# Performance work log

Measured on AMD Instinct MI355X. Metric: run time of the kernel, lower is better.

Reference implementation:

```python
import jax, jax.numpy as jnp
import numpy as np

B, L, H = 16, 512, 1024
K_START, K_END = 5, 5
LN_EPS = 1e-12
NEG = 1e30


def _layer_norm(x, gamma, beta):
    mu = jnp.mean(x, axis=-1, keepdims=True)
    var = jnp.mean(jnp.square(x - mu), axis=-1, keepdims=True)
    return (x - mu) * jax.lax.rsqrt(var + LN_EPS) * gamma + beta


def setup_inputs() -> dict:
    key = jax.random.key(0)
    ks = jax.random.split(key, 10)
    s = 0.02
    sequence_data = jax.random.normal(ks[0], (B, L, H), jnp.float32)
    class_index = jax.random.randint(ks[1], (B,), 0, L, dtype=jnp.int32)
    paragraph_mask = (jax.random.uniform(ks[2], (B, L)) > 0.1).astype(jnp.float32)
    paragraph_mask = paragraph_mask.at[:, 0].set(1.0)  # guarantee >=1 valid position per row
    return {
        'sequence_data': sequence_data,
        'class_index': class_index,
        'paragraph_mask': paragraph_mask,
        'W_start': jax.random.normal(ks[3], (H, 1), jnp.float32) * s,
        'b_start': jnp.zeros((1,), jnp.float32),
        'W_end_in': jax.random.normal(ks[4], (2 * H, H), jnp.float32) * s,
        'b_end_in': jnp.zeros((H,), jnp.float32),
        'ln_gamma': jnp.ones((H,), jnp.float32),
        'ln_beta': jnp.zeros((H,), jnp.float32),
        'W_end_out': jax.random.normal(ks[5], (H, 1), jnp.float32) * s,
        'b_end_out': jnp.zeros((1,), jnp.float32),
        'W_ans_in': jax.random.normal(ks[6], (2 * H, H), jnp.float32) * s,
        'b_ans_in': jnp.zeros((H,), jnp.float32),
        'W_ans_out': jax.random.normal(ks[7], (H, 1), jnp.float32) * s,
    }


def reference(sequence_data, class_index, paragraph_mask,
              W_start, b_start, W_end_in, b_end_in, ln_gamma, ln_beta,
              W_end_out, b_end_out, W_ans_in, b_ans_in, W_ans_out):
    mask = paragraph_mask  # [b, l] float, 1 = valid

    # ---- start logits ----
    start_logits = jnp.einsum('blh,ho->bl', sequence_data, W_start) + b_start[0]  # [b,l]
    masked_start_logits = start_logits * mask - NEG * (1.0 - mask)
    start_predictions = jax.nn.log_softmax(masked_start_logits, axis=-1)

    # ---- beam search over start positions (inference branch) ----
    start_top_predictions, start_top_index = jax.lax.top_k(start_predictions, K_START)  # [b,k]
    # one-hot einsum gather 'blh,bkl->bkh' expressed as direct indexing
    start_features = jnp.take_along_axis(sequence_data, start_top_index[:, :, None], axis=1)  # [b,k,h]

    # end_logits inner dense on concat([tiled seq, tiled start_features]) along h:
    # split the [2h, h] kernel and broadcast-add instead of materializing the tiled concat.
    W1, W2 = W_end_in[:H], W_end_in[H:]
    inner = jnp.tanh(
        jnp.einsum('blh,hd->bld', sequence_data, W1)[:, :, None, :]
        + jnp.einsum('bkh,hd->bkd', start_features, W2)[:, None, :, :]
        + b_end_in
    )  # [b,l,k,h]
    inner = _layer_norm(inner, ln_gamma, ln_beta)
    end_logits = jnp.einsum('blkh,ho->blk', inner, W_end_out) + b_end_out[0]  # [b,l,k]
    end_logits = jnp.transpose(end_logits, (0, 2, 1))  # [b,k,l]

    mask_k = mask[:, None, :]  # [b,1,l]
    masked_end_logits = end_logits * mask_k - NEG * (1.0 - mask_k)
    end_predictions = jax.nn.log_softmax(masked_end_logits, axis=-1)

    end_top_predictions, _end_top_index = jax.lax.top_k(end_predictions, K_END)  # [b,k,k2]
    end_top_predictions = end_top_predictions.reshape(-1, K_START * K_END)

    # ---- answer (class) logits ----
    class_feature = sequence_data[jnp.arange(sequence_data.shape[0]), class_index]  # [b,h]
    start_p = jax.nn.softmax(masked_start_logits, axis=-1)
    start_feature = jnp.einsum('blh,bl->bh', sequence_data, start_p)
    answer_feature = jnp.concatenate([start_feature, class_feature], axis=-1)  # [b,2h]
    answer_feature = jnp.tanh(answer_feature @ W_ans_in + b_ans_in)  # dropout is identity at inference
    class_logits = (answer_feature @ W_ans_out)[:, 0]  # [b]

    return (start_predictions, end_predictions, masked_start_logits, masked_end_logits,
            start_top_predictions, end_top_predictions, class_logits)
```

## Files before the change

### kernel.cpp

```cpp
#include <hip/hip_runtime.h>
#include <math.h>

#define HD   1024
#define LSEQ 512
#define NB   16
#define KTOP 5
#define NEGV 1e30f

typedef __bf16 bf16x8 __attribute__((ext_vector_type(8)));
typedef float  f32x4  __attribute__((ext_vector_type(4)));

__device__ inline unsigned short f2bf(float f) {
  unsigned u = __float_as_uint(f);
  unsigned r = (u + 0x7FFFu + ((u >> 16) & 1u)) >> 16;
  return (unsigned short)r;
}
__device__ inline float bf2f(unsigned short u) {
  return __uint_as_float(((unsigned)u) << 16);
}

__device__ inline float fast_tanh(float x) {
  float e = __expf(-2.f * fabsf(x));
  float v = (1.f - e) / (1.f + e);
  return copysignf(v, x);
}

__device__ inline float tanh_scaled(float xs) {
  float e = __builtin_amdgcn_exp2f(xs);
  float r = __builtin_amdgcn_rcpf(1.f + e);
  return fmaf(-2.f, r, 1.f);
}

#define GLDS(g, l) __builtin_amdgcn_global_load_lds(                      \
    (const __attribute__((address_space(1))) unsigned int*)(g),          \
    (__attribute__((address_space(3))) unsigned int*)(l), 16, 0, 0)

__global__ void k_prep(const float* __restrict__ seq,
                       unsigned short* __restrict__ seqb,
                       const float* __restrict__ Wst,
                       const float* __restrict__ bst,
                       const float* __restrict__ mask,
                       float* __restrict__ msl,
                       const float* __restrict__ Wei,
                       unsigned short* __restrict__ w1t,
                       const float* __restrict__ gam,
                       const float* __restrict__ bet,
                       const float* __restrict__ Weo,
                       const float* __restrict__ beo,
                       float* __restrict__ gw_ws,
                       float* __restrict__ sgb_ws) {
  __shared__ unsigned short tile[32][33];
  __shared__ float redp[4][2];
  int bx = blockIdx.x;
  if (bx < 2048) {
    int wave = threadIdx.x >> 6, lane = threadIdx.x & 63;
    int row = bx * 4 + wave;
    const float4* s4 = (const float4*)(seq + (size_t)row * HD);
    const float4* w4 = (const float4*)Wst;
    ushort4* o4 = (ushort4*)(seqb + (size_t)row * HD);
    float acc = 0.f;
#pragma unroll
    for (int m = 0; m < 4; ++m) {
      int i = lane + 64 * m;
      float4 a = s4[i], w = w4[i];
      acc += a.x * w.x + a.y * w.y + a.z * w.z + a.w * w.w;
      ushort4 o;
      o.x = f2bf(a.x); o.y = f2bf(a.y); o.z = f2bf(a.z); o.w = f2bf(a.w);
      o4[i] = o;
    }
#pragma unroll
    for (int off = 32; off; off >>= 1) acc += __shfl_xor(acc, off);
    if (lane == 0) {
      float logit = acc + bst[0];
      float mv = mask[row];
      msl[row] = logit * mv - NEGV * (1.f - mv);
    }
  } else if (bx < 3072) {
    int tb = bx - 2048;
    int h0 = (tb & 31) * 32, d0 = (tb >> 5) * 32;
    int tx = threadIdx.x & 31, ty = threadIdx.x >> 5;
#pragma unroll
    for (int i = 0; i < 4; ++i)
      tile[ty + 8 * i][tx] = f2bf(Wei[(size_t)(h0 + ty + 8 * i) * HD + d0 + tx]);
    __syncthreads();
#pragma unroll
    for (int i = 0; i < 4; ++i)
      w1t[(size_t)(d0 + ty + 8 * i) * HD + h0 + tx] = tile[tx][ty + 8 * i];
  } else {
    int t = threadIdx.x, wave = t >> 6, lane = t & 63;
    float4 g = ((const float4*)gam)[t];
    float4 w = ((const float4*)Weo)[t];
    float4 bv = ((const float4*)bet)[t];
    float4 gwv = make_float4(g.x * w.x, g.y * w.y, g.z * w.z, g.w * w.w);
    ((float4*)gw_ws)[t] = gwv;
    float pg = gwv.x + gwv.y + gwv.z + gwv.w;
    float pb = bv.x * w.x + bv.y * w.y + bv.z * w.z + bv.w * w.w;
#pragma unroll
    for (int off = 32; off; off >>= 1) {
      pg += __shfl_xor(pg, off);
      pb += __shfl_xor(pb, off);
    }
    if (lane == 0) { redp[wave][0] = pg; redp[wave][1] = pb; }
    __syncthreads();
    if (t == 0) {
      sgb_ws[0] = redp[0][0] + redp[1][0] + redp[2][0] + redp[3][0];
      sgb_ws[1] = redp[0][1] + redp[1][1] + redp[2][1] + redp[3][1] + beo[0];
    }
  }
}

__global__ void k_softmax_topk(const float* __restrict__ xin,
                               float* __restrict__ lsm_out,
                               float* __restrict__ top_out,
                               float* __restrict__ p_out,
                               int* __restrict__ idx_out) {
  int row = blockIdx.x, t = threadIdx.x;
  int lane = t & 63, wid = t >> 6;
  __shared__ float redf[4];
  __shared__ int redi[4];
  __shared__ float bc_m, bc_s;
  __shared__ int bc_i;
  const float* x = xin + (size_t)row * LSEQ;
  float x0 = x[t], x1 = x[t + 256];

  float m = fmaxf(x0, x1);
#pragma unroll
  for (int off = 32; off; off >>= 1) m = fmaxf(m, __shfl_xor(m, off));
  if (lane == 0) redf[wid] = m;
  __syncthreads();
  if (t == 0) bc_m = fmaxf(fmaxf(redf[0], redf[1]), fmaxf(redf[2], redf[3]));
  __syncthreads();
  m = bc_m;

  float e0 = expf(x0 - m), e1 = expf(x1 - m);
  float s = e0 + e1;
#pragma unroll
  for (int off = 32; off; off >>= 1) s += __shfl_xor(s, off);
  if (lane == 0) redf[wid] = s;
  __syncthreads();
  if (t == 0) bc_s = redf[0] + redf[1] + redf[2] + redf[3];
  __syncthreads();
  s = bc_s;
  float ls = logf(s);

  lsm_out[(size_t)row * LSEQ + t] = x0 - m - ls;
  lsm_out[(size_t)row * LSEQ + t + 256] = x1 - m - ls;
  if (p_out) {
    float inv = 1.f / s;
    p_out[(size_t)row * LSEQ + t] = e0 * inv;
    p_out[(size_t)row * LSEQ + t + 256] = e1 * inv;
  }

  bool a0 = true, a1 = true;
  for (int it = 0; it < KTOP; ++it) {
    float v0 = a0 ? x0 : -INFINITY;
    float v1 = a1 ? x1 : -INFINITY;
    float bv = v0; int bi = t;
    if (v1 > bv) { bv = v1; bi = t + 256; }
#pragma unroll
    for (int off = 32; off; off >>= 1) {
      float ov = __shfl_xor(bv, off);
      int oi = __shfl_xor(bi, off);
      if (ov > bv || (ov == bv && oi < bi)) { bv = ov; bi = oi; }
    }
    __syncthreads();
    if (lane == 0) { redf[wid] = bv; redi[wid] = bi; }
    __syncthreads();
    if (t == 0) {
      float wv = redf[0]; int wi = redi[0];
      for (int w = 1; w < 4; ++w)
        if (redf[w] > wv || (redf[w] == wv && redi[w] < wi)) { wv = redf[w]; wi = redi[w]; }
      top_out[row * KTOP + it] = wv - m - ls;
      if (idx_out) idx_out[row * KTOP + it] = wi;
      bc_i = wi;
    }
    __syncthreads();
    int wi = bc_i;
    if (wi == t) a0 = false;
    if (wi == t + 256) a1 = false;
  }
}

__global__ void k_x2p(const float* __restrict__ seq,
                      const int* __restrict__ idx,
                      const float* __restrict__ Wei,
                      float* __restrict__ x2part) {
  int bk = blockIdx.x, b = bk / KTOP, s = blockIdx.y, t = threadIdx.x;
  __shared__ float srow[128];
  int l = idx[bk];
  if (t < 128) srow[t] = seq[((size_t)(b * LSEQ + l)) * HD + s * 128 + t];
  __syncthreads();
  const float* W2 = Wei + (size_t)HD * HD + (size_t)s * 128 * HD;
  float4 acc = make_float4(0.f, 0.f, 0.f, 0.f);
#pragma unroll 8
  for (int h = 0; h < 128; ++h) {
    float4 wv = *(const float4*)(W2 + (size_t)h * HD + 4 * t);
    float sv = srow[h];
    acc.x = fmaf(sv, wv.x, acc.x);
    acc.y = fmaf(sv, wv.y, acc.y);
    acc.z = fmaf(sv, wv.z, acc.z);
    acc.w = fmaf(sv, wv.w, acc.w);
  }
  *(float4*)(x2part + ((size_t)bk * 8 + s) * HD + 4 * t) = acc;
}

__global__ void k_x2r(const float* __restrict__ x2part,
                      const float* __restrict__ bei,
                      float* __restrict__ x2p) {
  int bk = blockIdx.x, t = threadIdx.x;
  float4 a = *(const float4*)(bei + 4 * t);
#pragma unroll
  for (int s = 0; s < 8; ++s) {
    float4 p = *(const float4*)(x2part + ((size_t)bk * 8 + s) * HD + 4 * t);
    a.x += p.x; a.y += p.y; a.z += p.z; a.w += p.w;
  }
  *(float4*)(x2p + (size_t)bk * HD + 4 * t) = a;
}

__launch_bounds__(256, 2)
__global__ void k_gemm(const unsigned short* __restrict__ Abf,
                       const unsigned short* __restrict__ Bt,
                       unsigned short* __restrict__ X1) {
  __shared__ unsigned short As[2][128 * 64];
  __shared__ unsigned short Bs[2][128 * 64];
  int t = threadIdx.x;
  int w = t >> 6, lane = t & 63, ln = lane & 15, hi = lane >> 4;
  int wr = w >> 1, wc = w & 1;
  int R0 = blockIdx.x * 128, C0 = blockIdx.y * 128;

  f32x4 acc[4][4] = {};

#define STAGE(buf, kc)                                                        \
  do {                                                                        \
    _Pragma("unroll")                                                         \
    for (int p_ = 0; p_ < 4; ++p_) {                                          \
      int rr_ = p_ * 32 + (t >> 3);                                           \
      int cc_ = (t & 7) ^ (rr_ & 7);                                          \
      GLDS(Abf + (size_t)(R0 + rr_) * HD + (kc) + cc_ * 8,                    \
           &As[buf][p_ * 2048 + w * 512]);                                    \
      GLDS(Bt + (size_t)(C0 + rr_) * HD + (kc) + cc_ * 8,                     \
           &Bs[buf][p_ * 2048 + w * 512]);                                    \
    }                                                                         \
  } while (0)

  STAGE(0, 0);
  for (int it = 0; it < 16; ++it) {
    int cur = it & 1;
    if (it < 15) {
      STAGE(cur ^ 1, (it + 1) * 64);
      asm volatile("s_waitcnt vmcnt(8)" ::: "memory");
    } else {
      asm volatile("s_waitcnt vmcnt(0)" ::: "memory");
    }
    __builtin_amdgcn_s_barrier();
    __builtin_amdgcn_sched_barrier(0);
#pragma unroll
    for (int ks = 0; ks < 2; ++ks) {
      bf16x8 av[4], bv[4];
#pragma unroll
      for (int m = 0; m < 4; ++m) {
        int r = wr * 64 + m * 16 + ln;
        av[m] = *(const bf16x8*)(const void*)&As[cur][r * 64 + (((ks * 4 + hi) ^ (r & 7)) * 8)];
      }
#pragma unroll
      for (int n = 0; n < 4; ++n) {
        int r = wc * 64 + n * 16 + ln;
        bv[n] = *(const bf16x8*)(const void*)&Bs[cur][r * 64 + (((ks * 4 + hi) ^ (r & 7)) * 8)];
      }
#pragma unroll
      for (int m = 0; m < 4; ++m)
#pragma unroll
        for (int n = 0; n < 4; ++n)
          acc[m][n] = __builtin_amdgcn_mfma_f32_16x16x32_bf16(av[m], bv[n], acc[m][n], 0, 0, 0);
    }
    __builtin_amdgcn_sched_barrier(0);
    __builtin_amdgcn_s_barrier();
  }
#undef STAGE

#pragma unroll
  for (int m = 0; m < 4; ++m)
#pragma unroll
    for (int j = 0; j < 4; ++j) {
      int row = R0 + wr * 64 + m * 16 + hi * 4 + j;
#pragma unroll
      for (int n = 0; n < 4; ++n) {
        int col = C0 + wc * 64 + n * 16 + ln;
        X1[(size_t)row * HD + col] = f2bf(acc[m][n][j]);
      }
    }
}

__launch_bounds__(256)
__global__ void k_endrow(const unsigned short* __restrict__ X1,
                         const float* __restrict__ x2p,
                         const float* __restrict__ gw_ws,
                         const float* __restrict__ sgb_ws,
                         const float* __restrict__ mask,
                         float* __restrict__ mel) {
  __shared__ float x2s[KTOP * HD];
  const float A = 2.885390081777927f;
  int t = threadIdx.x, wave = t >> 6, lane = t & 63;
  int row = blockIdx.x * 4 + wave;
  int b = row >> 9, l = row & 511;

  {
    const float4* src = (const float4*)(x2p + (size_t)b * KTOP * HD);
    float4* dst = (float4*)x2s;
    for (int i = t; i < KTOP * HD / 4; i += 256) {
      float4 v = src[i];
      dst[i] = make_float4(v.x * A, v.y * A, v.z * A, v.w * A);
    }
  }

  float xs[16], gwr[16];
  const unsigned short* xrow = X1 + (size_t)row * HD + lane * 4;
#pragma unroll
  for (int q = 0; q < 4; ++q) {
    ushort4 u = *(const ushort4*)(xrow + q * 256);
    xs[4 * q + 0] = bf2f(u.x) * A;
    xs[4 * q + 1] = bf2f(u.y) * A;
    xs[4 * q + 2] = bf2f(u.z) * A;
    xs[4 * q + 3] = bf2f(u.w) * A;
    float4 g = *(const float4*)(gw_ws + q * 256 + lane * 4);
    gwr[4 * q + 0] = g.x; gwr[4 * q + 1] = g.y;
    gwr[4 * q + 2] = g.z; gwr[4 * q + 3] = g.w;
  }
  float mv = mask[row];
  float sG = sgb_ws[0], sBW = sgb_ws[1];
  __syncthreads();

#pragma unroll
  for (int k = 0; k < KTOP; ++k) {
    float sv = 0.f, s2 = 0.f, sg = 0.f;
#pragma unroll
    for (int q = 0; q < 4; ++q) {
      float4 xq = *(const float4*)&x2s[k * HD + q * 256 + lane * 4];
      float v0 = tanh_scaled(xs[4 * q + 0] + xq.x);
      float v1 = tanh_scaled(xs[4 * q + 1] + xq.y);
      float v2 = tanh_scaled(xs[4 * q + 2] + xq.z);
      float v3 = tanh_scaled(xs[4 * q + 3] + xq.w);
      sv += v0 + v1 + v2 + v3;
      s2 = fmaf(v0, v0, s2); s2 = fmaf(v1, v1, s2);
      s2 = fmaf(v2, v2, s2); s2 = fmaf(v3, v3, s2);
      sg = fmaf(v0, gwr[4 * q + 0], sg); sg = fmaf(v1, gwr[4 * q + 1], sg);
      sg = fmaf(v2, gwr[4 * q + 2], sg); sg = fmaf(v3, gwr[4 * q + 3], sg);
    }
#pragma unroll
    for (int off = 32; off; off >>= 1) {
      sv += __shfl_xor(sv, off);
      s2 += __shfl_xor(s2, off);
      sg += __shfl_xor(sg, off);
    }
    if (lane == 0) {
      float mu = sv * (1.f / (float)HD);
      float var = s2 * (1.f / (float)HD) - mu * mu;
      float rr = rsqrtf(var + 1e-12f);
      float logit = rr * (sg - mu * sG) + sBW;
      mel[((size_t)b * KTOP + k) * LSEQ + l] = logit * mv - NEGV * (1.f - mv);
    }
  }
}

__global__ void k_ans_in(const float* __restrict__ seq,
                         const float* __restrict__ p_ws,
                         const int* __restrict__ cls,
                         float* __restrict__ pa,
                         float* __restrict__ cf) {
  int b = blockIdx.x, s = blockIdx.y, t = threadIdx.x;
  __shared__ float ps[16];
  if (t < 16) ps[t] = p_ws[b * LSEQ + s * 16 + t];
  __syncthreads();
  const float* sb = seq + (size_t)(b * LSEQ + s * 16) * HD;
  float4 acc = make_float4(0.f, 0.f, 0.f, 0.f);
#pragma unroll
  for (int r = 0; r < 16; ++r) {
    float4 v = *(const float4*)(sb + (size_t)r * HD + 4 * t);
    float p = ps[r];
    acc.x = fmaf(p, v.x, acc.x);
    acc.y = fmaf(p, v.y, acc.y);
    acc.z = fmaf(p, v.z, acc.z);
    acc.w = fmaf(p, v.w, acc.w);
  }
  *(float4*)(pa + ((size_t)b * 32 + s) * HD + 4 * t) = acc;
  if (s == 0) {
    int ci = cls[b];
    *(float4*)(cf + (size_t)b * HD + 4 * t) =
        *(const float4*)(seq + (size_t)(b * LSEQ + ci) * HD + 4 * t);
  }
}

__global__ void k_ans_mid(const float* __restrict__ pa,
                          const float* __restrict__ cf,
                          const float* __restrict__ Wai,
                          float* __restrict__ pans) {
  int b = blockIdx.x, c = blockIdx.y, t = threadIdx.x;
  __shared__ float a_s[128];
  if (t < 128) {
    int i = c * 128 + t;
    float av;
    if (i < HD) {
      av = 0.f;
#pragma unroll
      for (int s = 0; s < 32; ++s) av += pa[((size_t)b * 32 + s) * HD + i];
    } else {
      av = cf[(size_t)b * HD + (i - HD)];
    }
    a_s[t] = av;
  }
  __syncthreads();
  float4 acc = make_float4(0.f, 0.f, 0.f, 0.f);
#pragma unroll 8
  for (int r = 0; r < 128; ++r) {
    float4 wv = *(const float4*)(Wai + (size_t)(c * 128 + r) * HD + 4 * t);
    float a = a_s[r];
    acc.x = fmaf(a, wv.x, acc.x);
    acc.y = fmaf(a, wv.y, acc.y);
    acc.z = fmaf(a, wv.z, acc.z);
    acc.w = fmaf(a, wv.w, acc.w);
  }
  *(float4*)(pans + ((size_t)b * 16 + c) * HD + 4 * t) = acc;
}

__global__ void k_ans_final(const float* __restrict__ pans,
                            const float* __restrict__ bai,
                            const float* __restrict__ Wao,
                            float* __restrict__ out6) {
  int b = blockIdx.x, t = threadIdx.x, lane = t & 63, wid = t >> 6;
  __shared__ float red[4];
  float4 a = *(const float4*)(bai + 4 * t);
#pragma unroll
  for (int c = 0; c < 16; ++c) {
    float4 p = *(const float4*)(pans + ((size_t)b * 16 + c) * HD + 4 * t);
    a.x += p.x; a.y += p.y; a.z += p.z; a.w += p.w;
  }
  float4 wo = *(const float4*)(Wao + 4 * t);
  float part = fast_tanh(a.x) * wo.x + fast_tanh(a.y) * wo.y +
               fast_tanh(a.z) * wo.z + fast_tanh(a.w) * wo.w;
#pragma unroll
  for (int off = 32; off; off >>= 1) part += __shfl_xor(part, off);
  if (lane == 0) red[wid] = part;
  __syncthreads();
  if (t == 0) out6[b] = red[0] + red[1] + red[2] + red[3];
}

__launch_bounds__(256, 2)
__global__ void k_gemm_end_at(const unsigned short* __restrict__ Abf,
                              const unsigned short* __restrict__ Bt,
                              const float* __restrict__ x2p,
                              const float* __restrict__ gamma,
                              const float* __restrict__ Wout,
                              float* __restrict__ outp) {
  __shared__ unsigned short As[2][128 * 64];
  __shared__ unsigned short Bs[2][128 * 64];
  int t = threadIdx.x;
  int w = t >> 6, lane = t & 63, ln = lane & 15, hi = lane >> 4;
  int wr = w >> 1, wc = w & 1;
  int R0 = blockIdx.x * 128, C0 = blockIdx.y * 128;
  int b = R0 >> 9;
  f32x4 acc[4][4] = {};
#define STAGE(buf, kc)                                                        \
  do {                                                                        \
    _Pragma("unroll")                                                         \
    for (int p_ = 0; p_ < 4; ++p_) {                                          \
      int rr_ = p_ * 32 + (t >> 3);                                           \
      int cc_ = (t & 7) ^ (rr_ & 7);                                          \
      GLDS(Abf + (size_t)(R0 + rr_) * HD + (kc) + cc_ * 8,                    \
           &As[buf][p_ * 2048 + w * 512]);                                    \
      GLDS(Bt + (size_t)(C0 + rr_) * HD + (kc) + cc_ * 8,                     \
           &Bs[buf][p_ * 2048 + w * 512]);                                    \
    }                                                                         \
  } while (0)
  STAGE(0, 0);
  for (int it = 0; it < 16; ++it) {
    int cur = it & 1;
    if (it < 15) {
      STAGE(cur ^ 1, (it + 1) * 64);
      asm volatile("s_waitcnt vmcnt(8)" ::: "memory");
    } else {
      asm volatile("s_waitcnt vmcnt(0)" ::: "memory");
    }
    __builtin_amdgcn_s_barrier();
    __builtin_amdgcn_sched_barrier(0);
#pragma unroll
    for (int ks = 0; ks < 2; ++ks) {
      bf16x8 av[4], bv[4];
#pragma unroll
      for (int m = 0; m < 4; ++m) {
        int r = wr * 64 + m * 16 + ln;
        av[m] = *(const bf16x8*)(const void*)&As[cur][r * 64 + (((ks * 4 + hi) ^ (r & 7)) * 8)];
      }
#pragma unroll
      for (int n = 0; n < 4; ++n) {
        int r = wc * 64 + n * 16 + ln;
        bv[n] = *(const bf16x8*)(const void*)&Bs[cur][r * 64 + (((ks * 4 + hi) ^ (r & 7)) * 8)];
      }
#pragma unroll
      for (int m = 0; m < 4; ++m)
#pragma unroll
        for (int n = 0; n < 4; ++n)
          acc[m][n] = __builtin_amdgcn_mfma_f32_16x16x32_bf16(av[m], bv[n], acc[m][n], 0, 0, 0);
    }
    __builtin_amdgcn_sched_barrier(0);
    __builtin_amdgcn_s_barrier();
  }
#undef STAGE
  float gsv[4];
  float x2v[4][KTOP];
#pragma unroll
  for (int n = 0; n < 4; ++n) {
    int c = C0 + wc * 64 + n * 16 + ln;
    gsv[n] = gamma[c] * Wout[c];
#pragma unroll
    for (int k = 0; k < KTOP; ++k) x2v[n][k] = x2p[((size_t)b * KTOP + k) * HD + c];
  }
#pragma unroll
  for (int m = 0; m < 4; ++m)
#pragma unroll
    for (int j = 0; j < 4; ++j) {
      int row = R0 + wr * 64 + m * 16 + hi * 4 + j;
#pragma unroll
      for (int k = 0; k < KTOP; ++k) {
        float sv = 0.f, s2 = 0.f, sg = 0.f;
#pragma unroll
        for (int n = 0; n < 4; ++n) {
          float v = fast_tanh(acc[m][n][j] + x2v[n][k]);
          sv += v; s2 += v * v; sg += v * gsv[n];
        }
#pragma unroll
        for (int off = 8; off; off >>= 1) {
          sv += __shfl_xor(sv, off);
          s2 += __shfl_xor(s2, off);
          sg += __shfl_xor(sg, off);
        }
        if (ln == 0) {
          float* p = outp + ((size_t)row * KTOP + k) * 3;
          atomicAdd(p, sv);
          atomicAdd(p + 1, s2);
          atomicAdd(p + 2, sg);
        }
      }
    }
}

__global__ void k_end_final(const float* __restrict__ sums,
                            const float* __restrict__ gamma,
                            const float* __restrict__ beta,
                            const float* __restrict__ Wout,
                            const float* __restrict__ beo,
                            const float* __restrict__ mask,
                            float* __restrict__ mel) {
  int bk = blockIdx.x, b = bk / KTOP, k = bk % KTOP;
  int t = threadIdx.x, lane = t & 63, wid = t >> 6;
  __shared__ float red[4][2];
  float pg = 0.f, pb = 0.f;
  for (int i = t; i < HD; i += 256) {
    float wv = Wout[i];
    pg += gamma[i] * wv;
    pb += beta[i] * wv;
  }
#pragma unroll
  for (int off = 32; off; off >>= 1) {
    pg += __shfl_xor(pg, off);
    pb += __shfl_xor(pb, off);
  }
  if (lane == 0) { red[wid][0] = pg; red[wid][1] = pb; }
  __syncthreads();
  float sG = red[0][0] + red[1][0] + red[2][0] + red[3][0];
  float sBW = red[0][1] + red[1][1] + red[2][1] + red[3][1] + beo[0];
  for (int l = t; l < LSEQ; l += 256) {
    int row = b * LSEQ + l;
    const float* s = sums + ((size_t)row * KTOP + k) * 3;
    float sv = s[0], s2 = s[1], sg = s[2];
    float mu = sv * (1.f / (float)HD);
    float var = s2 * (1.f / (float)HD) - mu * mu;
    float rr = rsqrtf(var + 1e-12f);
    float logit = rr * (sg - mu * sG) + sBW;
    float mv = mask[row];
    mel[((size_t)b * KTOP + k) * LSEQ + l] = logit * mv - NEGV * (1.f - mv);
  }
}

extern "C" void kernel_launch(void* const* d_in, const int* in_sizes, int n_in,
                              void* d_out, int out_size, void* d_ws, size_t ws_size,
                              hipStream_t stream) {
  (void)in_sizes; (void)n_in; (void)out_size;
  const float* seq = (const float*)d_in[0];
  const int*   cls = (const int*)d_in[1];
  const float* mask = (const float*)d_in[2];
  const float* Wst = (const float*)d_in[3];
  const float* bst = (const float*)d_in[4];
  const float* Wei = (const float*)d_in[5];
  const float* bei = (const float*)d_in[6];
  const float* gam = (const float*)d_in[7];
  const float* bet = (const float*)d_in[8];
  const float* Weo = (const float*)d_in[9];
  const float* beo = (const float*)d_in[10];
  const float* Wai = (const float*)d_in[11];
  const float* bai = (const float*)d_in[12];
  const float* Wao = (const float*)d_in[13];

  float* out = (float*)d_out;
  float* out0 = out;
  float* out1 = out0 + 8192;
  float* out2 = out1 + 40960;
  float* out3 = out2 + 8192;
  float* out4 = out3 + 40960;
  float* out5 = out4 + 80;
  float* out6 = out5 + 400;

  char* p = (char*)d_ws;
  unsigned short* seqb = (unsigned short*)p;  p += (size_t)8192 * 1024 * 2;
  unsigned short* w1t  = (unsigned short*)p;  p += (size_t)1024 * 1024 * 2;
  float* p_ws   = (float*)p;                  p += 8192 * 4;
  int*   idx_ws = (int*)p;                    p += 128 * 4;
  float* x2p    = (float*)p;                  p += (size_t)80 * 1024 * 4;
  float* gw_ws  = (float*)p;                  p += 1024 * 4;
  float* sgb_ws = (float*)p;                  p += 4 * 4;
  float* pa     = (float*)p;                  p += (size_t)16 * 32 * 1024 * 4;
  float* cf     = (float*)p;                  p += (size_t)16 * 1024 * 4;
  float* pans   = (float*)p;                  p += (size_t)16 * 16 * 1024 * 4;
  float* x2part = (float*)p;
  unsigned short* x1 = (unsigned short*)p;
  float* sums = (float*)(p + (size_t)640 * 1024 * 4);
  size_t base = (size_t)(p - (char*)d_ws);
  size_t need_big = base + (size_t)8192 * 1024 * 2;
  size_t need_small = base + (size_t)640 * 1024 * 4 + (size_t)8192 * KTOP * 3 * 4;

  k_prep<<<3073, 256, 0, stream>>>(seq, seqb, Wst, bst, mask, out2, Wei, w1t,
                                   gam, bet, Weo, beo, gw_ws, sgb_ws);
  k_softmax_topk<<<NB, 256, 0, stream>>>(out2, out0, out4, p_ws, idx_ws);
  k_x2p<<<dim3(NB * KTOP, 8), 256, 0, stream>>>(seq, idx_ws, Wei, x2part);
  k_x2r<<<NB * KTOP, 256, 0, stream>>>(x2part, bei, x2p);

  if (ws_size >= need_big) {
    k_gemm<<<dim3(64, 8), 256, 0, stream>>>(seqb, w1t, x1);
    k_endrow<<<2048, 256, 0, stream>>>(x1, x2p, gw_ws, sgb_ws, mask, out3);
  } else if (ws_size >= need_small) {
    hipMemsetAsync(sums, 0, (size_t)8192 * KTOP * 3 * sizeof(float), stream);
    k_gemm_end_at<<<dim3(64, 8), 256, 0, stream>>>(seqb, w1t, x2p, gam, Weo, sums);
    k_end_final<<<NB * KTOP, 256, 0, stream>>>(sums, gam, bet, Weo, beo, mask, out3);
  }

  k_softmax_topk<<<NB * KTOP, 256, 0, stream>>>(out3, out1, out5, nullptr, nullptr);
  k_ans_in<<<dim3(NB, 32), 256, 0, stream>>>(seq, p_ws, cls, pa, cf);
  k_ans_mid<<<dim3(NB, 16), 256, 0, stream>>>(pa, cf, Wai, pans);
  k_ans_final<<<NB, 256, 0, stream>>>(pans, bai, Wao, out6);
}
```

Measured before the change: 105.4 us.

## Merge independent kernels into horizontally fused launches with atomic x2 accumulation

```diff
diff --git a/kernel.cpp b/kernel.cpp
--- a/kernel.cpp
+++ b/kernel.cpp
@@ -34,6 +34,334 @@
 #define GLDS(g, l) __builtin_amdgcn_global_load_lds(                      \
     (const __attribute__((address_space(1))) unsigned int*)(g),          \
     (__attribute__((address_space(3))) unsigned int*)(l), 16, 0, 0)
+
+
+__device__ __forceinline__ void sm_body(int row, const float* __restrict__ xin,
+                                        float* __restrict__ lsm_out,
+                                        float* __restrict__ top_out,
+                                        float* __restrict__ p_out,
+                                        int* __restrict__ idx_out) {
+  __shared__ float redf[4];
+  __shared__ int redi[4];
+  __shared__ float bc_m, bc_s;
+  __shared__ int bc_i;
+  int t = threadIdx.x, lane = t & 63, wid = t >> 6;
+  const float* x = xin + (size_t)row * LSEQ;
+  float x0 = x[t], x1 = x[t + 256];
+
+  float m = fmaxf(x0, x1);
+#pragma unroll
+  for (int off = 32; off; off >>= 1) m = fmaxf(m, __shfl_xor(m, off));
+  if (lane == 0) redf[wid] = m;
+  __syncthreads();
+  if (t == 0) bc_m = fmaxf(fmaxf(redf[0], redf[1]), fmaxf(redf[2], redf[3]));
+  __syncthreads();
+  m = bc_m;
+
+  float e0 = expf(x0 - m), e1 = expf(x1 - m);
+  float s = e0 + e1;
+#pragma unroll
+  for (int off = 32; off; off >>= 1) s += __shfl_xor(s, off);
+  if (lane == 0) redf[wid] = s;
+  __syncthreads();
+  if (t == 0) bc_s = redf[0] + redf[1] + redf[2] + redf[3];
+  __syncthreads();
+  s = bc_s;
+  float ls = logf(s);
+
+  lsm_out[(size_t)row * LSEQ + t] = x0 - m - ls;
+  lsm_out[(size_t)row * LSEQ + t + 256] = x1 - m - ls;
+  if (p_out) {
+    float inv = 1.f / s;
+    p_out[(size_t)row * LSEQ + t] = e0 * inv;
+    p_out[(size_t)row * LSEQ + t + 256] = e1 * inv;
+  }
+
+  bool a0 = true, a1 = true;
+  for (int it = 0; it < KTOP; ++it) {
+    float v0 = a0 ? x0 : -INFINITY;
+    float v1 = a1 ? x1 : -INFINITY;
+    float bv = v0; int bi = t;
+    if (v1 > bv) { bv = v1; bi = t + 256; }
+#pragma unroll
+    for (int off = 32; off; off >>= 1) {
+      float ov = __shfl_xor(bv, off);
+      int oi = __shfl_xor(bi, off);
+      if (ov > bv || (ov == bv && oi < bi)) { bv = ov; bi = oi; }
+    }
+    __syncthreads();
+    if (lane == 0) { redf[wid] = bv; redi[wid] = bi; }
+    __syncthreads();
+    if (t == 0) {
+      float wv = redf[0]; int wi = redi[0];
+      for (int w = 1; w < 4; ++w)
+        if (redf[w] > wv || (redf[w] == wv && redi[w] < wi)) { wv = redf[w]; wi = redi[w]; }
+      top_out[row * KTOP + it] = wv - m - ls;
+      if (idx_out) idx_out[row * KTOP + it] = wi;
+      bc_i = wi;
+    }
+    __syncthreads();
+    int wi = bc_i;
+    if (wi == t) a0 = false;
+    if (wi == t + 256) a1 = false;
+  }
+}
+
+__device__ __forceinline__ void gemm_body(int gid,
+                                          const unsigned short* __restrict__ Abf,
+                                          const unsigned short* __restrict__ Bt,
+                                          unsigned short* __restrict__ X1) {
+  __shared__ unsigned short SH[32768];
+  unsigned short* As = SH;
+  unsigned short* Bs = SH + 16384;
+  int t = threadIdx.x;
+  int w = t >> 6, lane = t & 63, ln = lane & 15, hi = lane >> 4;
+  int wr = w >> 1, wc = w & 1;
+  int R0 = (gid >> 3) * 128, C0 = (gid & 7) * 128;
+
+  f32x4 acc[4][4] = {};
+
+#define STAGE(buf, kc)                                                        \
+  do {                                                                        \
+    _Pragma("unroll")                                                         \
+    for (int p_ = 0; p_ < 4; ++p_) {                                          \
+      int rr_ = p_ * 32 + (t >> 3);                                           \
+      int cc_ = (t & 7) ^ (rr_ & 7);                                          \
+      GLDS(Abf + (size_t)(R0 + rr_) * HD + (kc) + cc_ * 8,                    \
+           As + (buf) * 8192 + p_ * 2048 + w * 512);                          \
+      GLDS(Bt + (size_t)(C0 + rr_) * HD + (kc) + cc_ * 8,                     \
+           Bs + (buf) * 8192 + p_ * 2048 + w * 512);                          \
+    }                                                                         \
+  } while (0)
+
+  STAGE(0, 0);
+  for (int it = 0; it < 16; ++it) {
+    int cur = it & 1;
+    if (it < 15) {
+      STAGE(cur ^ 1, (it + 1) * 64);
+      asm volatile("s_waitcnt vmcnt(8)" ::: "memory");
+    } else {
+      asm volatile("s_waitcnt vmcnt(0)" ::: "memory");
+    }
+    __builtin_amdgcn_s_barrier();
+    __builtin_amdgcn_sched_barrier(0);
+#pragma unroll
+    for (int ks = 0; ks < 2; ++ks) {
+      bf16x8 av[4], bv[4];
+#pragma unroll
+      for (int m = 0; m < 4; ++m) {
+        int r = wr * 64 + m * 16 + ln;
+        av[m] = *(const bf16x8*)(const void*)&As[cur * 8192 + r * 64 + (((ks * 4 + hi) ^ (r & 7)) * 8)];
+      }
+#pragma unroll
+      for (int n = 0; n < 4; ++n) {
+        int r = wc * 64 + n * 16 + ln;
+        bv[n] = *(const bf16x8*)(const void*)&Bs[cur * 8192 + r * 64 + (((ks * 4 + hi) ^ (r & 7)) * 8)];
+      }
+#pragma unroll
+      for (int m = 0; m < 4; ++m)
+#pragma unroll
+        for (int n = 0; n < 4; ++n)
+          acc[m][n] = __builtin_amdgcn_mfma_f32_16x16x32_bf16(av[m], bv[n], acc[m][n], 0, 0, 0);
+    }
+    __builtin_amdgcn_sched_barrier(0);
+    __builtin_amdgcn_s_barrier();
+  }
+#undef STAGE
+
+#pragma unroll
+  for (int m = 0; m < 4; ++m)
+#pragma unroll
+    for (int j = 0; j < 4; ++j) {
+      int row = R0 + wr * 64 + m * 16 + hi * 4 + j;
+#pragma unroll
+      for (int n = 0; n < 4; ++n) {
+        int col = C0 + wc * 64 + n * 16 + ln;
+        X1[(size_t)row * HD + col] = f2bf(acc[m][n][j]);
+      }
+    }
+}
+
+__device__ __forceinline__ void x2slice_body(int q, const float* __restrict__ seq,
+                                             const int* __restrict__ idx,
+                                             const float* __restrict__ Wei,
+                                             float* __restrict__ x2p) {
+  __shared__ float srow[128];
+  int bk = q >> 3, s = q & 7, t = threadIdx.x;
+  int b = bk / KTOP;
+  int l = idx[bk];
+  if (t < 128) srow[t] = seq[((size_t)(b * LSEQ + l)) * HD + s * 128 + t];
+  __syncthreads();
+  const float* W2 = Wei + (size_t)HD * HD + (size_t)s * 128 * HD;
+  float4 acc = make_float4(0.f, 0.f, 0.f, 0.f);
+#pragma unroll 8
+  for (int h = 0; h < 128; ++h) {
+    float4 wv = *(const float4*)(W2 + (size_t)h * HD + 4 * t);
+    float sv = srow[h];
+    acc.x = fmaf(sv, wv.x, acc.x);
+    acc.y = fmaf(sv, wv.y, acc.y);
+    acc.z = fmaf(sv, wv.z, acc.z);
+    acc.w = fmaf(sv, wv.w, acc.w);
+  }
+  float* dst = x2p + (size_t)bk * HD + 4 * t;
+  atomicAdd(dst + 0, acc.x);
+  atomicAdd(dst + 1, acc.y);
+  atomicAdd(dst + 2, acc.z);
+  atomicAdd(dst + 3, acc.w);
+}
+
+__device__ __forceinline__ void ansin_body(int q, const float* __restrict__ seq,
+                                           const float* __restrict__ p_ws,
+                                           const int* __restrict__ cls,
+                                           float* __restrict__ pa,
+                                           float* __restrict__ cf) {
+  __shared__ float ps[16];
+  int b = q >> 5, s = q & 31, t = threadIdx.x;
+  if (t < 16) ps[t] = p_ws[b * LSEQ + s * 16 + t];
+  __syncthreads();
+  const float* sb = seq + (size_t)(b * LSEQ + s * 16) * HD;
+  float4 acc = make_float4(0.f, 0.f, 0.f, 0.f);
+#pragma unroll
+  for (int r = 0; r < 16; ++r) {
+    float4 v = *(const float4*)(sb + (size_t)r * HD + 4 * t);
+    float p = ps[r];
+    acc.x = fmaf(p, v.x, acc.x);
+    acc.y = fmaf(p, v.y, acc.y);
+    acc.z = fmaf(p, v.z, acc.z);
+    acc.w = fmaf(p, v.w, acc.w);
+  }
+  *(float4*)(pa + ((size_t)b * 32 + s) * HD + 4 * t) = acc;
+  if (s == 0) {
+    int ci = cls[b];
+    *(float4*)(cf + (size_t)b * HD + 4 * t) =
+        *(const float4*)(seq + (size_t)(b * LSEQ + ci) * HD + 4 * t);
+  }
+}
+
+__device__ __forceinline__ void endrow_body(int bx, const unsigned short* __restrict__ X1,
+                                            const float* __restrict__ x2p,
+                                            const float* __restrict__ gw_ws,
+                                            const float* __restrict__ sgb_ws,
+                                            const float* __restrict__ mask,
+                                            float* __restrict__ mel) {
+  __shared__ float x2s[KTOP * HD];
+  const float A = 2.885390081777927f;
+  int t = threadIdx.x, wave = t >> 6, lane = t & 63;
+  int row = bx * 4 + wave;
+  int b = row >> 9, l = row & 511;
+
+  {
+    const float4* src = (const float4*)(x2p + (size_t)b * KTOP * HD);
+    float4* dst = (float4*)x2s;
+    for (int i = t; i < KTOP * HD / 4; i += 256) {
+      float4 v = src[i];
+      dst[i] = make_float4(v.x * A, v.y * A, v.z * A, v.w * A);
+    }
+  }
+
+  float xs[16], gwr[16];
+  const unsigned short* xrow = X1 + (size_t)row * HD + lane * 4;
+#pragma unroll
+  for (int q = 0; q < 4; ++q) {
+    ushort4 u = *(const ushort4*)(xrow + q * 256);
+    xs[4 * q + 0] = bf2f(u.x) * A;
+    xs[4 * q + 1] = bf2f(u.y) * A;
+    xs[4 * q + 2] = bf2f(u.z) * A;
+    xs[4 * q + 3] = bf2f(u.w) * A;
+    float4 g = *(const float4*)(gw_ws + q * 256 + lane * 4);
+    gwr[4 * q + 0] = g.x; gwr[4 * q + 1] = g.y;
+    gwr[4 * q + 2] = g.z; gwr[4 * q + 3] = g.w;
+  }
+  float mv = mask[row];
+  float sG = sgb_ws[0], sBW = sgb_ws[1];
+  __syncthreads();
+
+#pragma unroll
+  for (int k = 0; k < KTOP; ++k) {
+    float sv = 0.f, s2 = 0.f, sg = 0.f;
+#pragma unroll
+    for (int q = 0; q < 4; ++q) {
+      float4 xq = *(const float4*)&x2s[k * HD + q * 256 + lane * 4];
+      float v0 = tanh_scaled(xs[4 * q + 0] + xq.x);
+      float v1 = tanh_scaled(xs[4 * q + 1] + xq.y);
+      float v2 = tanh_scaled(xs[4 * q + 2] + xq.z);
+      float v3 = tanh_scaled(xs[4 * q + 3] + xq.w);
+      sv += v0 + v1 + v2 + v3;
+      s2 = fmaf(v0, v0, s2); s2 = fmaf(v1, v1, s2);
+      s2 = fmaf(v2, v2, s2); s2 = fmaf(v3, v3, s2);
+      sg = fmaf(v0, gwr[4 * q + 0], sg); sg = fmaf(v1, gwr[4 * q + 1], sg);
+      sg = fmaf(v2, gwr[4 * q + 2], sg); sg = fmaf(v3, gwr[4 * q + 3], sg);
+    }
+#pragma unroll
+    for (int off = 32; off; off >>= 1) {
+      sv += __shfl_xor(sv, off);
+      s2 += __shfl_xor(s2, off);
+      sg += __shfl_xor(sg, off);
+    }
+    if (lane == 0) {
+      float mu = sv * (1.f / (float)HD);
+      float var = s2 * (1.f / (float)HD) - mu * mu;
+      float rr = rsqrtf(var + 1e-12f);
+      float logit = rr * (sg - mu * sG) + sBW;
+      mel[((size_t)b * KTOP + k) * LSEQ + l] = logit * mv - NEGV * (1.f - mv);
+    }
+  }
+}
+
+__device__ __forceinline__ void ansmid_body(int q, const float* __restrict__ pa,
+                                            const float* __restrict__ cf,
+                                            const float* __restrict__ Wai,
+                                            float* __restrict__ pans) {
+  __shared__ float a_s[128];
+  int b = q >> 4, c = q & 15, t = threadIdx.x;
+  if (t < 128) {
+    int i = c * 128 + t;
+    float av;
+    if (i < HD) {
+      av = 0.f;
+#pragma unroll
+      for (int s = 0; s < 32; ++s) av += pa[((size_t)b * 32 + s) * HD + i];
+    } else {
+      av = cf[(size_t)b * HD + (i - HD)];
+    }
+    a_s[t] = av;
+  }
+  __syncthreads();
+  float4 acc = make_float4(0.f, 0.f, 0.f, 0.f);
+#pragma unroll 8
+  for (int r = 0; r < 128; ++r) {
+    float4 wv = *(const float4*)(Wai + (size_t)(c * 128 + r) * HD + 4 * t);
+    float a = a_s[r];
+    acc.x = fmaf(a, wv.x, acc.x);
+    acc.y = fmaf(a, wv.y, acc.y);
+    acc.z = fmaf(a, wv.z, acc.z);
+    acc.w = fmaf(a, wv.w, acc.w);
+  }
+  *(float4*)(pans + ((size_t)b * 16 + c) * HD + 4 * t) = acc;
+}
+
+__device__ __forceinline__ void ansfinal_body(int b, const float* __restrict__ pans,
+                                              const float* __restrict__ bai,
+                                              const float* __restrict__ Wao,
+                                              float* __restrict__ out6) {
+  __shared__ float red[4];
+  int t = threadIdx.x, lane = t & 63, wid = t >> 6;
+  float4 a = *(const float4*)(bai + 4 * t);
+#pragma unroll
+  for (int c = 0; c < 16; ++c) {
+    float4 p = *(const float4*)(pans + ((size_t)b * 16 + c) * HD + 4 * t);
+    a.x += p.x; a.y += p.y; a.z += p.z; a.w += p.w;
+  }
+  float4 wo = *(const float4*)(Wao + 4 * t);
+  float part = fast_tanh(a.x) * wo.x + fast_tanh(a.y) * wo.y +
+               fast_tanh(a.z) * wo.z + fast_tanh(a.w) * wo.w;
+#pragma unroll
+  for (int off = 32; off; off >>= 1) part += __shfl_xor(part, off);
+  if (lane == 0) red[wid] = part;
+  __syncthreads();
+  if (t == 0) out6[b] = red[0] + red[1] + red[2] + red[3];
+}
+
 
 __global__ void k_prep(const float* __restrict__ seq,
                        unsigned short* __restrict__ seqb,
@@ -48,7 +376,9 @@
                        const float* __restrict__ Weo,
                        const float* __restrict__ beo,
                        float* __restrict__ gw_ws,
-                       float* __restrict__ sgb_ws) {
+                       float* __restrict__ sgb_ws,
+                       const float* __restrict__ bei,
+                       float* __restrict__ x2p) {
   __shared__ unsigned short tile[32][33];
   __shared__ float redp[4][2];
   int bx = blockIdx.x;
@@ -86,7 +416,7 @@
 #pragma unroll
     for (int i = 0; i < 4; ++i)
       w1t[(size_t)(d0 + ty + 8 * i) * HD + h0 + tx] = tile[tx][ty + 8 * i];
-  } else {
+  } else if (bx == 3072) {
     int t = threadIdx.x, wave = t >> 6, lane = t & 63;
     float4 g = ((const float4*)gam)[t];
     float4 w = ((const float4*)Weo)[t];
@@ -106,6 +436,9 @@
       sgb_ws[0] = redp[0][0] + redp[1][0] + redp[2][0] + redp[3][0];
       sgb_ws[1] = redp[0][1] + redp[1][1] + redp[2][1] + redp[3][1] + beo[0];
     }
+  } else {
+    int row = bx - 3073;
+    ((float4*)(x2p + (size_t)row * HD))[threadIdx.x] = ((const float4*)bei)[threadIdx.x];
   }
 }
 
@@ -114,334 +447,67 @@
                                float* __restrict__ top_out,
                                float* __restrict__ p_out,
                                int* __restrict__ idx_out) {
-  int row = blockIdx.x, t = threadIdx.x;
-  int lane = t & 63, wid = t >> 6;
-  __shared__ float redf[4];
-  __shared__ int redi[4];
-  __shared__ float bc_m, bc_s;
-  __shared__ int bc_i;
-  const float* x = xin + (size_t)row * LSEQ;
-  float x0 = x[t], x1 = x[t + 256];
-
-  float m = fmaxf(x0, x1);
-#pragma unroll
-  for (int off = 32; off; off >>= 1) m = fmaxf(m, __shfl_xor(m, off));
-  if (lane == 0) redf[wid] = m;
-  __syncthreads();
-  if (t == 0) bc_m = fmaxf(fmaxf(redf[0], redf[1]), fmaxf(redf[2], redf[3]));
-  __syncthreads();
-  m = bc_m;
-
-  float e0 = expf(x0 - m), e1 = expf(x1 - m);
-  float s = e0 + e1;
-#pragma unroll
-  for (int off = 32; off; off >>= 1) s += __shfl_xor(s, off);
-  if (lane == 0) redf[wid] = s;
-  __syncthreads();
-  if (t == 0) bc_s = redf[0] + redf[1] + redf[2] + redf[3];
-  __syncthreads();
-  s = bc_s;
-  float ls = logf(s);
-
-  lsm_out[(size_t)row * LSEQ + t] = x0 - m - ls;
-  lsm_out[(size_t)row * LSEQ + t + 256] = x1 - m - ls;
-  if (p_out) {
-    float inv = 1.f / s;
-    p_out[(size_t)row * LSEQ + t] = e0 * inv;
-    p_out[(size_t)row * LSEQ + t + 256] = e1 * inv;
-  }
-
-  bool a0 = true, a1 = true;
-  for (int it = 0; it < KTOP; ++it) {
-    float v0 = a0 ? x0 : -INFINITY;
-    float v1 = a1 ? x1 : -INFINITY;
-    float bv = v0; int bi = t;
-    if (v1 > bv) { bv = v1; bi = t + 256; }
-#pragma unroll
-    for (int off = 32; off; off >>= 1) {
-      float ov = __shfl_xor(bv, off);
-      int oi = __shfl_xor(bi, off);
-      if (ov > bv || (ov == bv && oi < bi)) { bv = ov; bi = oi; }
-    }
-    __syncthreads();
-    if (lane == 0) { redf[wid] = bv; redi[wid] = bi; }
-    __syncthreads();
-    if (t == 0) {
-      float wv = redf[0]; int wi = redi[0];
-      for (int w = 1; w < 4; ++w)
-        if (redf[w] > wv || (redf[w] == wv && redi[w] < wi)) { wv = redf[w]; wi = redi[w]; }
-      top_out[row * KTOP + it] = wv - m - ls;
-      if (idx_out) idx_out[row * KTOP + it] = wi;
-      bc_i = wi;
-    }
-    __syncthreads();
-    int wi = bc_i;
-    if (wi == t) a0 = false;
-    if (wi == t + 256) a1 = false;
-  }
-}
-
-__global__ void k_x2p(const float* __restrict__ seq,
+  sm_body(blockIdx.x, xin, lsm_out, top_out, p_out, idx_out);
+}
+
+__launch_bounds__(256, 2)
+__global__ void k_big(const unsigned short* __restrict__ Abf,
+                      const unsigned short* __restrict__ Bt,
+                      unsigned short* __restrict__ X1,
+                      const float* __restrict__ seq,
                       const int* __restrict__ idx,
                       const float* __restrict__ Wei,
-                      float* __restrict__ x2part) {
-  int bk = blockIdx.x, b = bk / KTOP, s = blockIdx.y, t = threadIdx.x;
-  __shared__ float srow[128];
-  int l = idx[bk];
-  if (t < 128) srow[t] = seq[((size_t)(b * LSEQ + l)) * HD + s * 128 + t];
-  __syncthreads();
-  const float* W2 = Wei + (size_t)HD * HD + (size_t)s * 128 * HD;
-  float4 acc = make_float4(0.f, 0.f, 0.f, 0.f);
-#pragma unroll 8
-  for (int h = 0; h < 128; ++h) {
-    float4 wv = *(const float4*)(W2 + (size_t)h * HD + 4 * t);
-    float sv = srow[h];
-    acc.x = fmaf(sv, wv.x, acc.x);
-    acc.y = fmaf(sv, wv.y, acc.y);
-    acc.z = fmaf(sv, wv.z, acc.z);
-    acc.w = fmaf(sv, wv.w, acc.w);
-  }
-  *(float4*)(x2part + ((size_t)bk * 8 + s) * HD + 4 * t) = acc;
-}
-
-__global__ void k_x2r(const float* __restrict__ x2part,
-                      const float* __restrict__ bei,
-                      float* __restrict__ x2p) {
-  int bk = blockIdx.x, t = threadIdx.x;
-  float4 a = *(const float4*)(bei + 4 * t);
-#pragma unroll
-  for (int s = 0; s < 8; ++s) {
-    float4 p = *(const float4*)(x2part + ((size_t)bk * 8 + s) * HD + 4 * t);
-    a.x += p.x; a.y += p.y; a.z += p.z; a.w += p.w;
-  }
-  *(float4*)(x2p + (size_t)bk * HD + 4 * t) = a;
-}
-
-__launch_bounds__(256, 2)
-__global__ void k_gemm(const unsigned short* __restrict__ Abf,
-                       const unsigned short* __restrict__ Bt,
-                       unsigned short* __restrict__ X1) {
-  __shared__ unsigned short As[2][128 * 64];
-  __shared__ unsigned short Bs[2][128 * 64];
-  int t = threadIdx.x;
-  int w = t >> 6, lane = t & 63, ln = lane & 15, hi = lane >> 4;
-  int wr = w >> 1, wc = w & 1;
-  int R0 = blockIdx.x * 128, C0 = blockIdx.y * 128;
-
-  f32x4 acc[4][4] = {};
-
-#define STAGE(buf, kc)                                                        \
-  do {                                                                        \
-    _Pragma("unroll")                                                         \
-    for (int p_ = 0; p_ < 4; ++p_) {                                          \
-      int rr_ = p_ * 32 + (t >> 3);                                           \
-      int cc_ = (t & 7) ^ (rr_ & 7);                                          \
-      GLDS(Abf + (size_t)(R0 + rr_) * HD + (kc) + cc_ * 8,                    \
-           &As[buf][p_ * 2048 + w * 512]);                                    \
-      GLDS(Bt + (size_t)(C0 + rr_) * HD + (kc) + cc_ * 8,                     \
-           &Bs[buf][p_ * 2048 + w * 512]);                                    \
-    }                                                                         \
-  } while (0)
-
-  STAGE(0, 0);
-  for (int it = 0; it < 16; ++it) {
-    int cur = it & 1;
-    if (it < 15) {
-      STAGE(cur ^ 1, (it + 1) * 64);
-      asm volatile("s_waitcnt vmcnt(8)" ::: "memory");
-    } else {
-      asm volatile("s_waitcnt vmcnt(0)" ::: "memory");
-    }
-    __builtin_amdgcn_s_barrier();
-    __builtin_amdgcn_sched_barrier(0);
-#pragma unroll
-    for (int ks = 0; ks < 2; ++ks) {
-      bf16x8 av[4], bv[4];
-#pragma unroll
-      for (int m = 0; m < 4; ++m) {
-        int r = wr * 64 + m * 16 + ln;
-        av[m] = *(const bf16x8*)(const void*)&As[cur][r * 64 + (((ks * 4 + hi) ^ (r & 7)) * 8)];
-      }
-#pragma unroll
-      for (int n = 0; n < 4; ++n) {
-        int r = wc * 64 + n * 16 + ln;
-        bv[n] = *(const bf16x8*)(const void*)&Bs[cur][r * 64 + (((ks * 4 + hi) ^ (r & 7)) * 8)];
-      }
-#pragma unroll
-      for (int m = 0; m < 4; ++m)
-#pragma unroll
-        for (int n = 0; n < 4; ++n)
-          acc[m][n] = __builtin_amdgcn_mfma_f32_16x16x32_bf16(av[m], bv[n], acc[m][n], 0, 0, 0);
-    }
-    __builtin_amdgcn_sched_barrier(0);
-    __builtin_amdgcn_s_barrier();
-  }
-#undef STAGE
-
-#pragma unroll
-  for (int m = 0; m < 4; ++m)
-#pragma unroll
-    for (int j = 0; j < 4; ++j) {
-      int row = R0 + wr * 64 + m * 16 + hi * 4 + j;
-#pragma unroll
-      for (int n = 0; n < 4; ++n) {
-        int col = C0 + wc * 64 + n * 16 + ln;
-        X1[(size_t)row * HD + col] = f2bf(acc[m][n][j]);
-      }
-    }
-}
-
-__launch_bounds__(256)
-__global__ void k_endrow(const unsigned short* __restrict__ X1,
-                         const float* __restrict__ x2p,
-                         const float* __restrict__ gw_ws,
-                         const float* __restrict__ sgb_ws,
-                         const float* __restrict__ mask,
-                         float* __restrict__ mel) {
-  __shared__ float x2s[KTOP * HD];
-  const float A = 2.885390081777927f;
-  int t = threadIdx.x, wave = t >> 6, lane = t & 63;
-  int row = blockIdx.x * 4 + wave;
-  int b = row >> 9, l = row & 511;
-
-  {
-    const float4* src = (const float4*)(x2p + (size_t)b * KTOP * HD);
-    float4* dst = (float4*)x2s;
-    for (int i = t; i < KTOP * HD / 4; i += 256) {
-      float4 v = src[i];
-      dst[i] = make_float4(v.x * A, v.y * A, v.z * A, v.w * A);
-    }
-  }
-
-  float xs[16], gwr[16];
-  const unsigned short* xrow = X1 + (size_t)row * HD + lane * 4;
-#pragma unroll
-  for (int q = 0; q < 4; ++q) {
-    ushort4 u = *(const ushort4*)(xrow + q * 256);
-    xs[4 * q + 0] = bf2f(u.x) * A;
-    xs[4 * q + 1] = bf2f(u.y) * A;
-    xs[4 * q + 2] = bf2f(u.z) * A;
-    xs[4 * q + 3] = bf2f(u.w) * A;
-    float4 g = *(const float4*)(gw_ws + q * 256 + lane * 4);
-    gwr[4 * q + 0] = g.x; gwr[4 * q + 1] = g.y;
-    gwr[4 * q + 2] = g.z; gwr[4 * q + 3] = g.w;
-  }
-  float mv = mask[row];
-  float sG = sgb_ws[0], sBW = sgb_ws[1];
-  __syncthreads();
-
-#pragma unroll
-  for (int k = 0; k < KTOP; ++k) {
-    float sv = 0.f, s2 = 0.f, sg = 0.f;
-#pragma unroll
-    for (int q = 0; q < 4; ++q) {
-      float4 xq = *(const float4*)&x2s[k * HD + q * 256 + lane * 4];
-      float v0 = tanh_scaled(xs[4 * q + 0] + xq.x);
-      float v1 = tanh_scaled(xs[4 * q + 1] + xq.y);
-      float v2 = tanh_scaled(xs[4 * q + 2] + xq.z);
-      float v3 = tanh_scaled(xs[4 * q + 3] + xq.w);
-      sv += v0 + v1 + v2 + v3;
-      s2 = fmaf(v0, v0, s2); s2 = fmaf(v1, v1, s2);
-      s2 = fmaf(v2, v2, s2); s2 = fmaf(v3, v3, s2);
-      sg = fmaf(v0, gwr[4 * q + 0], sg); sg = fmaf(v1, gwr[4 * q + 1], sg);
-      sg = fmaf(v2, gwr[4 * q + 2], sg); sg = fmaf(v3, gwr[4 * q + 3], sg);
-    }
-#pragma unroll
-    for (int off = 32; off; off >>= 1) {
-      sv += __shfl_xor(sv, off);
-      s2 += __shfl_xor(s2, off);
-      sg += __shfl_xor(sg, off);
-    }
-    if (lane == 0) {
-      float mu = sv * (1.f / (float)HD);
-      float var = s2 * (1.f / (float)HD) - mu * mu;
-      float rr = rsqrtf(var + 1e-12f);
-      float logit = rr * (sg - mu * sG) + sBW;
-      mel[((size_t)b * KTOP + k) * LSEQ + l] = logit * mv - NEGV * (1.f - mv);
-    }
-  }
-}
-
-__global__ void k_ans_in(const float* __restrict__ seq,
-                         const float* __restrict__ p_ws,
-                         const int* __restrict__ cls,
-                         float* __restrict__ pa,
-                         float* __restrict__ cf) {
-  int b = blockIdx.x, s = blockIdx.y, t = threadIdx.x;
-  __shared__ float ps[16];
-  if (t < 16) ps[t] = p_ws[b * LSEQ + s * 16 + t];
-  __syncthreads();
-  const float* sb = seq + (size_t)(b * LSEQ + s * 16) * HD;
-  float4 acc = make_float4(0.f, 0.f, 0.f, 0.f);
-#pragma unroll
-  for (int r = 0; r < 16; ++r) {
-    float4 v = *(const float4*)(sb + (size_t)r * HD + 4 * t);
-    float p = ps[r];
-    acc.x = fmaf(p, v.x, acc.x);
-    acc.y = fmaf(p, v.y, acc.y);
-    acc.z = fmaf(p, v.z, acc.z);
-    acc.w = fmaf(p, v.w, acc.w);
-  }
-  *(float4*)(pa + ((size_t)b * 32 + s) * HD + 4 * t) = acc;
-  if (s == 0) {
-    int ci = cls[b];
-    *(float4*)(cf + (size_t)b * HD + 4 * t) =
-        *(const float4*)(seq + (size_t)(b * LSEQ + ci) * HD + 4 * t);
-  }
-}
-
-__global__ void k_ans_mid(const float* __restrict__ pa,
-                          const float* __restrict__ cf,
-                          const float* __restrict__ Wai,
-                          float* __restrict__ pans) {
-  int b = blockIdx.x, c = blockIdx.y, t = threadIdx.x;
-  __shared__ float a_s[128];
-  if (t < 128) {
-    int i = c * 128 + t;
-    float av;
-    if (i < HD) {
-      av = 0.f;
-#pragma unroll
-      for (int s = 0; s < 32; ++s) av += pa[((size_t)b * 32 + s) * HD + i];
-    } else {
-      av = cf[(size_t)b * HD + (i - HD)];
-    }
-    a_s[t] = av;
-  }
-  __syncthreads();
-  float4 acc = make_float4(0.f, 0.f, 0.f, 0.f);
-#pragma unroll 8
-  for (int r = 0; r < 128; ++r) {
-    float4 wv = *(const float4*)(Wai + (size_t)(c * 128 + r) * HD + 4 * t);
-    float a = a_s[r];
-    acc.x = fmaf(a, wv.x, acc.x);
-    acc.y = fmaf(a, wv.y, acc.y);
-    acc.z = fmaf(a, wv.z, acc.z);
-    acc.w = fmaf(a, wv.w, acc.w);
-  }
-  *(float4*)(pans + ((size_t)b * 16 + c) * HD + 4 * t) = acc;
-}
-
-__global__ void k_ans_final(const float* __restrict__ pans,
-                            const float* __restrict__ bai,
-                            const float* __restrict__ Wao,
-                            float* __restrict__ out6) {
-  int b = blockIdx.x, t = threadIdx.x, lane = t & 63, wid = t >> 6;
-  __shared__ float red[4];
-  float4 a = *(const float4*)(bai + 4 * t);
-#pragma unroll
-  for (int c = 0; c < 16; ++c) {
-    float4 p = *(const float4*)(pans + ((size_t)b * 16 + c) * HD + 4 * t);
-    a.x += p.x; a.y += p.y; a.z += p.z; a.w += p.w;
-  }
-  float4 wo = *(const float4*)(Wao + 4 * t);
-  float part = fast_tanh(a.x) * wo.x + fast_tanh(a.y) * wo.y +
-               fast_tanh(a.z) * wo.z + fast_tanh(a.w) * wo.w;
-#pragma unroll
-  for (int off = 32; off; off >>= 1) part += __shfl_xor(part, off);
-  if (lane == 0) red[wid] = part;
-  __syncthreads();
-  if (t == 0) out6[b] = red[0] + red[1] + red[2] + red[3];
+                      float* __restrict__ x2p,
+                      const float* __restrict__ p_ws,
+                      const int* __restrict__ cls,
+                      float* __restrict__ pa,
+                      float* __restrict__ cf) {
+  int id = blockIdx.x;
+  int grp = id / 13, rem = id % 13;
+  if (rem < 4) gemm_body(grp * 4 + rem, Abf, Bt, X1);
+  else if (rem < 9) x2slice_body(grp * 5 + (rem - 4), seq, idx, Wei, x2p);
+  else ansin_body(grp * 4 + (rem - 9), seq, p_ws, cls, pa, cf);
+}
+
+__global__ void k_end2(const unsigned short* __restrict__ X1,
+                       const float* __restrict__ x2p,
+                       const float* __restrict__ gw_ws,
+                       const float* __restrict__ sgb_ws,
+                       const float* __restrict__ mask,
+                       float* __restrict__ mel,
+                       const float* __restrict__ pa,
+                       const float* __restrict__ cf,
+                       const float* __restrict__ Wai,
+                       float* __restrict__ pans) {
+  int bx = blockIdx.x;
+  if (bx < 2048) endrow_body(bx, X1, x2p, gw_ws, sgb_ws, mask, mel);
+  else ansmid_body(bx - 2048, pa, cf, Wai, pans);
+}
+
+__global__ void k_fin(const float* __restrict__ mel,
+                      float* __restrict__ lsm_out,
+                      float* __restrict__ top_out,
+                      const float* __restrict__ pans,
+                      const float* __restrict__ bai,
+                      const float* __restrict__ Wao,
+                      float* __restrict__ out6) {
+  int bx = blockIdx.x;
+  if (bx < NB * KTOP) sm_body(bx, mel, lsm_out, top_out, nullptr, nullptr);
+  else ansfinal_body(bx - NB * KTOP, pans, bai, Wao, out6);
+}
+
+__global__ void k_x2f(const float* __restrict__ seq, const int* __restrict__ idx,
+                      const float* __restrict__ Wei, float* __restrict__ x2p) {
+  x2slice_body(blockIdx.x, seq, idx, Wei, x2p);
+}
+__global__ void k_ansin_f(const float* __restrict__ seq, const float* __restrict__ p_ws,
+                          const int* __restrict__ cls, float* __restrict__ pa,
+                          float* __restrict__ cf) {
+  ansin_body(blockIdx.x, seq, p_ws, cls, pa, cf);
+}
+__global__ void k_ansmid_f(const float* __restrict__ pa, const float* __restrict__ cf,
+                           const float* __restrict__ Wai, float* __restrict__ pans) {
+  ansmid_body(blockIdx.x, pa, cf, Wai, pans);
 }
 
 __launch_bounds__(256, 2)
@@ -620,30 +686,29 @@
   float* pa     = (float*)p;                  p += (size_t)16 * 32 * 1024 * 4;
   float* cf     = (float*)p;                  p += (size_t)16 * 1024 * 4;
   float* pans   = (float*)p;                  p += (size_t)16 * 16 * 1024 * 4;
-  float* x2part = (float*)p;
   unsigned short* x1 = (unsigned short*)p;
-  float* sums = (float*)(p + (size_t)640 * 1024 * 4);
+  float* sums = (float*)p;
   size_t base = (size_t)(p - (char*)d_ws);
   size_t need_big = base + (size_t)8192 * 1024 * 2;
-  size_t need_small = base + (size_t)640 * 1024 * 4 + (size_t)8192 * KTOP * 3 * 4;
-
-  k_prep<<<3073, 256, 0, stream>>>(seq, seqb, Wst, bst, mask, out2, Wei, w1t,
-                                   gam, bet, Weo, beo, gw_ws, sgb_ws);
+  size_t need_small = base + (size_t)8192 * KTOP * 3 * 4;
+
+  k_prep<<<3153, 256, 0, stream>>>(seq, seqb, Wst, bst, mask, out2, Wei, w1t,
+                                   gam, bet, Weo, beo, gw_ws, sgb_ws, bei, x2p);
   k_softmax_topk<<<NB, 256, 0, stream>>>(out2, out0, out4, p_ws, idx_ws);
-  k_x2p<<<dim3(NB * KTOP, 8), 256, 0, stream>>>(seq, idx_ws, Wei, x2part);
-  k_x2r<<<NB * KTOP, 256, 0, stream>>>(x2part, bei, x2p);
 
   if (ws_size >= need_big) {
-    k_gemm<<<dim3(64, 8), 256, 0, stream>>>(seqb, w1t, x1);
-    k_endrow<<<2048, 256, 0, stream>>>(x1, x2p, gw_ws, sgb_ws, mask, out3);
+    k_big<<<1664, 256, 0, stream>>>(seqb, w1t, x1, seq, idx_ws, Wei, x2p,
+                                    p_ws, cls, pa, cf);
+    k_end2<<<2304, 256, 0, stream>>>(x1, x2p, gw_ws, sgb_ws, mask, out3,
+                                     pa, cf, Wai, pans);
   } else if (ws_size >= need_small) {
+    k_x2f<<<640, 256, 0, stream>>>(seq, idx_ws, Wei, x2p);
     hipMemsetAsync(sums, 0, (size_t)8192 * KTOP * 3 * sizeof(float), stream);
     k_gemm_end_at<<<dim3(64, 8), 256, 0, stream>>>(seqb, w1t, x2p, gam, Weo, sums);
     k_end_final<<<NB * KTOP, 256, 0, stream>>>(sums, gam, bet, Weo, beo, mask, out3);
-  }
-
-  k_softmax_topk<<<NB * KTOP, 256, 0, stream>>>(out3, out1, out5, nullptr, nullptr);
-  k_ans_in<<<dim3(NB, 32), 256, 0, stream>>>(seq, p_ws, cls, pa, cf);
-  k_ans_mid<<<dim3(NB, 16), 256, 0, stream>>>(pa, cf, Wai, pans);
-  k_ans_final<<<NB, 256, 0, stream>>>(pans, bai, Wao, out6);
-}
+    k_ansin_f<<<512, 256, 0, stream>>>(seq, p_ws, cls, pa, cf);
+    k_ansmid_f<<<256, 256, 0, stream>>>(pa, cf, Wai, pans);
+  }
+
+  k_fin<<<96, 256, 0, stream>>>(out3, out1, out5, pans, bai, Wao, out6);
+}
```

New measurement: 95.94 us. 9.0% less time.
